# Kernel optimization log

Hardware: AMD Instinct MI355X
Metric: run time of the kernel (lower is better)

## Reference

```python
import jax, jax.numpy as jnp
import numpy as np

N = 4096
IN_F = 256
F = 64      # out_features
H = 4       # heads
NEG_SLOPE = 0.2


def setup_inputs() -> dict:
    key = jax.random.key(0)
    k1, k2, k3, k4 = jax.random.split(key, 4)
    x = jax.random.normal(k1, (N, IN_F), dtype=jnp.float32)
    # symmetric random binary adjacency with self-loops (avoids empty softmax rows)
    adj = jax.random.bernoulli(k2, 0.5, (N, N)).astype(jnp.float32)
    adj = jnp.clip(adj + adj.T, 0.0, 1.0)
    adj = jnp.maximum(adj, jnp.eye(N, dtype=jnp.float32))
    W = jax.random.normal(k3, (IN_F, F * H), dtype=jnp.float32) * (1.0 / np.sqrt(IN_F))
    a = jax.random.normal(k4, (2 * F, 1), dtype=jnp.float32) * 0.1
    return {"x": x, "adj": adj, "W": W, "a": a}


def reference(x, adj, W, a):
    # h: [N, H, F]
    h = (x @ W).reshape(N, H, F)
    # e[i, j, h] = leakyrelu(a_l . h[i, h] + a_r . h[j, h])  -- avoids the O(N^2*H*2F) concat
    a_l = a[:F, 0]
    a_r = a[F:, 0]
    el = jnp.einsum('nhf,f->nh', h, a_l)  # [N, H]
    er = jnp.einsum('nhf,f->nh', h, a_r)  # [N, H]
    e = jax.nn.leaky_relu(el[:, None, :] + er[None, :, :], NEG_SLOPE)  # [N, N, H]
    e = jnp.where(adj[:, :, None] == 0, -jnp.inf, e)
    attention = jax.nn.softmax(e, axis=1)  # softmax over neighbors j
    h_prime = jnp.einsum('ijh,jhf->ihf', attention, h)  # [N, H, F]
    return h_prime.mean(axis=1)  # [N, F]  (heads > 1 -> mean over heads)
```

## Files before the change

kernel.cpp:

```cpp
#include <hip/hip_runtime.h>
#include <hip/hip_bf16.h>

#define NN 4096
#define LOG2E 1.44269504088896340736f
#define SPLITS 16

typedef __attribute__((ext_vector_type(8))) short s8v;
typedef __attribute__((ext_vector_type(4))) float f4v;

__device__ __forceinline__ unsigned fu(float x){ union{float f;unsigned u;}z; z.f=x; return z.u; }
__device__ __forceinline__ unsigned short f2bf_rne(float x){
  unsigned u = fu(x);
  u += 0x7fffu + ((u >> 16) & 1u);
  return (unsigned short)(u >> 16);
}
__device__ __forceinline__ unsigned pack2_rne(float a, float b){
  return (unsigned)f2bf_rne(a) | ((unsigned)f2bf_rne(b) << 16);
}

__global__ __launch_bounds__(256) void k1_proj(
    const float* __restrict__ x, const float* __restrict__ W,
    const float* __restrict__ a, unsigned short* __restrict__ Vf,
    float* __restrict__ el4, float* __restrict__ Qr, float* __restrict__ Sr)
{
  __shared__ float4 xs[512];
  const int t = threadIdx.x;
  const int r0 = blockIdx.x * 8;
  const float4* xg = (const float4*)(x + (size_t)r0 * 256);
  xs[t] = xg[t];
  xs[t + 256] = xg[t + 256];
  __syncthreads();

  float acc[8] = {0.f,0.f,0.f,0.f,0.f,0.f,0.f,0.f};
  const float* Wp = W + t;
  float w0 = Wp[0], w1 = Wp[256], w2 = Wp[512], w3 = Wp[768];
  #pragma unroll 1
  for (int k4 = 0; k4 < 64; ++k4) {
    const int kn = (k4 + 1) & 63;
    float nw0 = Wp[kn*1024 +   0];
    float nw1 = Wp[kn*1024 + 256];
    float nw2 = Wp[kn*1024 + 512];
    float nw3 = Wp[kn*1024 + 768];
    #pragma unroll
    for (int r = 0; r < 8; ++r) {
      float4 xv = xs[r*64 + k4];
      acc[r] = fmaf(xv.x, w0, acc[r]);
      acc[r] = fmaf(xv.y, w1, acc[r]);
      acc[r] = fmaf(xv.z, w2, acc[r]);
      acc[r] = fmaf(xv.w, w3, acc[r]);
    }
    w0 = nw0; w1 = nw1; w2 = nw2; w3 = nw3;
  }

  union { unsigned u[4]; s8v v; } pk;
  #pragma unroll
  for (int p = 0; p < 4; ++p)
    pk.u[p] = pack2_rne(acc[2*p], acc[2*p+1]);
  {
    const int hh = t >> 6, nf = (t >> 4) & 3, mm = t & 15;
    const int jblk = r0 >> 5, qq = (r0 >> 3) & 3;
    const size_t chunk = (size_t)(((hh * 128 + jblk) * 4 + nf) * 64 + qq * 16 + mm);
    *(s8v*)(Vf + chunk * 8) = pk.v;
  }

  const int f = t & 63, h = t >> 6;
  const float al = a[f], ar = a[64 + f];
  #pragma unroll
  for (int r = 0; r < 8; ++r) {
    float v = acc[r] * al;
    float u = acc[r] * ar;
    #pragma unroll
    for (int off = 32; off > 0; off >>= 1) {
      v += __shfl_xor(v, off);
      u += __shfl_xor(u, off);
    }
    if (f == 0) {
      el4[(r0 + r) * 4 + h] = v * LOG2E;
      float up = u * LOG2E;
      Qr[h * NN + (r0 + r)] = __builtin_amdgcn_exp2f(up);
      Sr[h * NN + (r0 + r)] = __builtin_amdgcn_exp2f(0.2f * up);
    }
  }
}

__global__ __launch_bounds__(256) void k0_pack(
    const float* __restrict__ adj, const float* __restrict__ el4,
    const float* __restrict__ Qr, const float* __restrict__ Sr,
    unsigned long long* __restrict__ adjP64,
    float* __restrict__ PL, float* __restrict__ RL)
{
  const int t = threadIdx.x;
  const int w = t >> 6, l = t & 63;
  const int row = blockIdx.x * 4 + w;
  const float* arow = adj + (size_t)row * NN;

  float4 elv = *(const float4*)(el4 + row * 4);
  const float P[4] = { __builtin_amdgcn_exp2f(elv.x), __builtin_amdgcn_exp2f(elv.y),
                       __builtin_amdgcn_exp2f(elv.z), __builtin_amdgcn_exp2f(elv.w) };
  const float R[4] = { __builtin_amdgcn_exp2f(0.2f*elv.x), __builtin_amdgcn_exp2f(0.2f*elv.y),
                       __builtin_amdgcn_exp2f(0.2f*elv.z), __builtin_amdgcn_exp2f(0.2f*elv.w) };
  float lsum[4] = {0.f, 0.f, 0.f, 0.f};

  float af[4], nf_[4];
  #pragma unroll
  for (int k = 0; k < 4; ++k) af[k] = arow[k * 64 + l];

  #pragma unroll 1
  for (int p = 0; p < 16; ++p) {
    const int nbase = (p < 15) ? (p + 1) * 256 : 0;
    #pragma unroll
    for (int k = 0; k < 4; ++k) nf_[k] = arow[nbase + k * 64 + l];

    const int base = p * 256;
    unsigned long long bm[4];
    #pragma unroll
    for (int k = 0; k < 4; ++k) {
      bm[k] = __ballot(af[k] != 0.0f);
      const int j = base + k * 64 + l;
      #pragma unroll
      for (int h = 0; h < 4; ++h) {
        float qv = Qr[h * NN + j];
        float sv = Sr[h * NN + j];
        lsum[h] = fmaf(af[k], fmaxf(P[h] * qv, R[h] * sv), lsum[h]);
      }
    }
    if (l == 0) {
      unsigned long long* dst = adjP64 + (size_t)row * 64 + p * 4;
      dst[0] = bm[0]; dst[1] = bm[1]; dst[2] = bm[2]; dst[3] = bm[3];
    }
    #pragma unroll
    for (int k = 0; k < 4; ++k) af[k] = nf_[k];
  }

  #pragma unroll
  for (int h = 0; h < 4; ++h) {
    float v = lsum[h];
    #pragma unroll
    for (int off = 32; off > 0; off >>= 1) v += __shfl_xor(v, off);
    lsum[h] = v;
  }
  if (l < 4) {
    float li = 1.0f / lsum[l];
    PL[row * 4 + l] = P[l] * li;
    RL[row * 4 + l] = R[l] * li;
  }
}

__global__ __launch_bounds__(256, 4) void k2_attn(
    const unsigned* __restrict__ adjP, const unsigned short* __restrict__ Vf,
    const float* __restrict__ PL, const float* __restrict__ RL,
    const float* __restrict__ Qr, const float* __restrict__ Sr,
    float* __restrict__ accF)
{
  __shared__ float qs[2048];
  const int t = threadIdx.x;
  const int w = t >> 6, l = t & 63;
  const int m = l & 15, q = l >> 4;
  const int i0 = blockIdx.x * 64;
  const int split = blockIdx.y;
  const int i = i0 + w * 16 + m;
  const int jwin = split * 256;

  {
    const int h = t >> 6;
    float4 qv = *(const float4*)(Qr + h * NN + jwin + l * 4);
    float4 sv = *(const float4*)(Sr + h * NN + jwin + l * 4);
    const int jc = l >> 3, qq = (l >> 1) & 3, hp = (l & 1) * 4;
    float* cell = qs + ((h * 8 + jc) * 4 + qq) * 16;
    *(float4*)(cell + hp) = qv;
    *(float4*)(cell + 8 + hp) = sv;
  }

  float4 pl4 = *(const float4*)(PL + i * 4);
  float4 rl4 = *(const float4*)(RL + i * 4);
  const float Pl[4] = {pl4.x, pl4.y, pl4.z, pl4.w};
  const float Rl[4] = {rl4.x, rl4.y, rl4.z, rl4.w};

  union { uint4 v[2]; unsigned u[8]; } aw;
  {
    const uint4* ap = (const uint4*)(adjP + (size_t)i * 128 + split * 8);
    aw.v[0] = ap[0];
    aw.v[1] = ap[1];
  }

  f4v acc[4];
  #pragma unroll
  for (int nf = 0; nf < 4; ++nf) acc[nf] = (f4v){0.f, 0.f, 0.f, 0.f};

  __syncthreads();

  #pragma unroll 1
  for (int jc = 0; jc < 8; ++jc) {
    const unsigned byte = (aw.u[jc] >> (q * 8)) & 0xFFu;
    float bitf[8];
    #pragma unroll
    for (int e = 0; e < 8; ++e)
      bitf[e] = (float)((byte >> e) & 1u);

    #pragma unroll
    for (int h = 0; h < 4; ++h) {
      const float* cell = qs + ((h * 8 + jc) * 4 + q) * 16;
      float4 q0  = *(const float4*)(cell);
      float4 q1  = *(const float4*)(cell + 4);
      float4 sv0 = *(const float4*)(cell + 8);
      float4 sv1 = *(const float4*)(cell + 12);
      const float Ph = Pl[h], Rh = Rl[h];
      float s0 = bitf[0] * fmaxf(Ph * q0.x, Rh * sv0.x);
      float s1 = bitf[1] * fmaxf(Ph * q0.y, Rh * sv0.y);
      float s2 = bitf[2] * fmaxf(Ph * q0.z, Rh * sv0.z);
      float s3 = bitf[3] * fmaxf(Ph * q0.w, Rh * sv0.w);
      float s4 = bitf[4] * fmaxf(Ph * q1.x, Rh * sv1.x);
      float s5 = bitf[5] * fmaxf(Ph * q1.y, Rh * sv1.y);
      float s6 = bitf[6] * fmaxf(Ph * q1.z, Rh * sv1.z);
      float s7 = bitf[7] * fmaxf(Ph * q1.w, Rh * sv1.w);
      union { unsigned u[4]; s8v v; } A;
      A.u[0] = pack2_rne(s0, s1);
      A.u[1] = pack2_rne(s2, s3);
      A.u[2] = pack2_rne(s4, s5);
      A.u[3] = pack2_rne(s6, s7);
      const s8v* vb = (const s8v*)Vf + ((size_t)((h * 128 + split * 8 + jc) * 4)) * 64 + l;
      #pragma unroll
      for (int nf = 0; nf < 4; ++nf) {
        s8v B = vb[nf * 64];
        acc[nf] = __builtin_amdgcn_mfma_f32_16x16x32_bf16(A.v, B, acc[nf], 0, 0, 0);
      }
    }
  }

  const size_t wbase = ((size_t)(split * 64 + blockIdx.x) * 4 + w) * 1024;
  #pragma unroll
  for (int nf = 0; nf < 4; ++nf)
    #pragma unroll
    for (int r = 0; r < 4; ++r)
      accF[wbase + (nf * 4 + r) * 64 + l] = acc[nf][r];
}

__global__ __launch_bounds__(256) void k3_reduce(
    const float* __restrict__ accF, float* __restrict__ out)
{
  const int pos = blockIdx.x * 256 + threadIdx.x;
  float s = 0.f;
  #pragma unroll
  for (int sp = 0; sp < SPLITS; ++sp)
    s += accF[(size_t)sp * 262144 + pos];
  const int l = pos & 63, r = (pos >> 6) & 3, nf = (pos >> 8) & 3;
  const int w = (pos >> 10) & 3, bx = pos >> 12;
  const int row = bx * 64 + w * 16 + (l >> 4) * 4 + r;
  const int col = nf * 16 + (l & 15);
  out[row * 64 + col] = 0.25f * s;
}

extern "C" void kernel_launch(void* const* d_in, const int* in_sizes, int n_in,
                              void* d_out, int out_size, void* d_ws, size_t ws_size,
                              hipStream_t stream) {
  const float* x   = (const float*)d_in[0];
  const float* adj = (const float*)d_in[1];
  const float* W   = (const float*)d_in[2];
  const float* a   = (const float*)d_in[3];
  float* out = (float*)d_out;

  char* ws = (char*)d_ws;
  unsigned short* Vf = (unsigned short*)ws;
  float* el4 = (float*)(ws + (2u << 20));
  float* Qr  = (float*)(ws + (2u << 20) + (64u << 10));
  float* Sr  = (float*)(ws + (2u << 20) + (128u << 10));
  float* PLp = (float*)(ws + (2u << 20) + (192u << 10));
  float* RLp = (float*)(ws + (2u << 20) + (256u << 10));
  unsigned long long* adjP64 = (unsigned long long*)(ws + (2u << 20) + (320u << 10));
  float* accF = (float*)(ws + (4u << 20) + (320u << 10));

  k1_proj<<<512, 256, 0, stream>>>(x, W, a, Vf, el4, Qr, Sr);
  k0_pack<<<1024, 256, 0, stream>>>(adj, el4, Qr, Sr, adjP64, PLp, RLp);
  k2_attn<<<dim3(64, SPLITS), 256, 0, stream>>>((const unsigned*)adjP64, Vf, PLp, RLp,
                                                Qr, Sr, accF);
  k3_reduce<<<1024, 256, 0, stream>>>(accF, out);
}
```

Baseline: 181.3 us.

## Vectorize adjacency packing, prefetch V fragments, replace split reduce with atomics

k0_pack now reads adjacency and Qr/Sr as float4 with one-iteration prefetch, so each 64-bit ballot covers strided columns and the packed bit layout changes. k2_attn decodes the new interleaved bit layout, software-pipelines the V fragment loads one step ahead of the MFMAs, and accumulates the scaled result directly into the output with atomicAdd. This removes the k3_reduce kernel and its partial-sum buffer in exchange for a memset and atomic contention across 16 splits, which also makes the float summation order nondeterministic.

```diff
diff --git a/kernel.cpp b/kernel.cpp
--- a/kernel.cpp
+++ b/kernel.cpp
@@ -83,10 +83,10 @@
   }
 }
 
-__global__ __launch_bounds__(256) void k0_pack(
+__global__ __launch_bounds__(256, 4) void k0_pack(
     const float* __restrict__ adj, const float* __restrict__ el4,
     const float* __restrict__ Qr, const float* __restrict__ Sr,
-    unsigned long long* __restrict__ adjP64,
+    unsigned long long* __restrict__ adjB,
     float* __restrict__ PL, float* __restrict__ RL)
 {
   const int t = threadIdx.x;
@@ -101,35 +101,54 @@
                        __builtin_amdgcn_exp2f(0.2f*elv.z), __builtin_amdgcn_exp2f(0.2f*elv.w) };
   float lsum[4] = {0.f, 0.f, 0.f, 0.f};
 
-  float af[4], nf_[4];
-  #pragma unroll
-  for (int k = 0; k < 4; ++k) af[k] = arow[k * 64 + l];
+  float4 av, qv0, qv1, qv2, qv3, sv0, sv1, sv2, sv3;
+  av  = *(const float4*)(arow + l * 4);
+  qv0 = *(const float4*)(Qr + 0 * NN + l * 4);
+  qv1 = *(const float4*)(Qr + 1 * NN + l * 4);
+  qv2 = *(const float4*)(Qr + 2 * NN + l * 4);
+  qv3 = *(const float4*)(Qr + 3 * NN + l * 4);
+  sv0 = *(const float4*)(Sr + 0 * NN + l * 4);
+  sv1 = *(const float4*)(Sr + 1 * NN + l * 4);
+  sv2 = *(const float4*)(Sr + 2 * NN + l * 4);
+  sv3 = *(const float4*)(Sr + 3 * NN + l * 4);
 
   #pragma unroll 1
   for (int p = 0; p < 16; ++p) {
-    const int nbase = (p < 15) ? (p + 1) * 256 : 0;
-    #pragma unroll
-    for (int k = 0; k < 4; ++k) nf_[k] = arow[nbase + k * 64 + l];
-
-    const int base = p * 256;
-    unsigned long long bm[4];
-    #pragma unroll
-    for (int k = 0; k < 4; ++k) {
-      bm[k] = __ballot(af[k] != 0.0f);
-      const int j = base + k * 64 + l;
-      #pragma unroll
-      for (int h = 0; h < 4; ++h) {
-        float qv = Qr[h * NN + j];
-        float sv = Sr[h * NN + j];
-        lsum[h] = fmaf(af[k], fmaxf(P[h] * qv, R[h] * sv), lsum[h]);
-      }
-    }
+    const int nb = ((p < 15) ? (p + 1) * 256 : 0) + l * 4;
+    float4 nav  = *(const float4*)(arow + nb);
+    float4 nqv0 = *(const float4*)(Qr + 0 * NN + nb);
+    float4 nqv1 = *(const float4*)(Qr + 1 * NN + nb);
+    float4 nqv2 = *(const float4*)(Qr + 2 * NN + nb);
+    float4 nqv3 = *(const float4*)(Qr + 3 * NN + nb);
+    float4 nsv0 = *(const float4*)(Sr + 0 * NN + nb);
+    float4 nsv1 = *(const float4*)(Sr + 1 * NN + nb);
+    float4 nsv2 = *(const float4*)(Sr + 2 * NN + nb);
+    float4 nsv3 = *(const float4*)(Sr + 3 * NN + nb);
+
+    unsigned long long b0 = __ballot(av.x != 0.0f);
+    unsigned long long b1 = __ballot(av.y != 0.0f);
+    unsigned long long b2 = __ballot(av.z != 0.0f);
+    unsigned long long b3 = __ballot(av.w != 0.0f);
     if (l == 0) {
-      unsigned long long* dst = adjP64 + (size_t)row * 64 + p * 4;
-      dst[0] = bm[0]; dst[1] = bm[1]; dst[2] = bm[2]; dst[3] = bm[3];
-    }
-    #pragma unroll
-    for (int k = 0; k < 4; ++k) af[k] = nf_[k];
+      unsigned long long* dst = adjB + (size_t)row * 64 + p * 4;
+      dst[0] = b0; dst[1] = b1; dst[2] = b2; dst[3] = b3;
+    }
+    #pragma unroll
+    for (int h = 0; h < 4; ++h) {
+      const float4 qv = (h==0)?qv0:(h==1)?qv1:(h==2)?qv2:qv3;
+      const float4 sv = (h==0)?sv0:(h==1)?sv1:(h==2)?sv2:sv3;
+      float m0 = fmaxf(P[h] * qv.x, R[h] * sv.x);
+      float m1 = fmaxf(P[h] * qv.y, R[h] * sv.y);
+      float m2 = fmaxf(P[h] * qv.z, R[h] * sv.z);
+      float m3 = fmaxf(P[h] * qv.w, R[h] * sv.w);
+      lsum[h] = fmaf(av.x, m0, lsum[h]);
+      lsum[h] = fmaf(av.y, m1, lsum[h]);
+      lsum[h] = fmaf(av.z, m2, lsum[h]);
+      lsum[h] = fmaf(av.w, m3, lsum[h]);
+    }
+    av = nav;
+    qv0 = nqv0; qv1 = nqv1; qv2 = nqv2; qv3 = nqv3;
+    sv0 = nsv0; sv1 = nsv1; sv2 = nsv2; sv3 = nsv3;
   }
 
   #pragma unroll
@@ -147,10 +166,10 @@
 }
 
 __global__ __launch_bounds__(256, 4) void k2_attn(
-    const unsigned* __restrict__ adjP, const unsigned short* __restrict__ Vf,
+    const unsigned long long* __restrict__ adjB, const unsigned short* __restrict__ Vf,
     const float* __restrict__ PL, const float* __restrict__ RL,
     const float* __restrict__ Qr, const float* __restrict__ Sr,
-    float* __restrict__ accF)
+    float* __restrict__ out)
 {
   __shared__ float qs[2048];
   const int t = threadIdx.x;
@@ -176,29 +195,43 @@
   const float Pl[4] = {pl4.x, pl4.y, pl4.z, pl4.w};
   const float Rl[4] = {rl4.x, rl4.y, rl4.z, rl4.w};
 
-  union { uint4 v[2]; unsigned u[8]; } aw;
-  {
-    const uint4* ap = (const uint4*)(adjP + (size_t)i * 128 + split * 8);
-    aw.v[0] = ap[0];
-    aw.v[1] = ap[1];
-  }
+  const unsigned long long* bp = adjB + (size_t)i * 64 + split * 4;
+  unsigned long long b0 = bp[0], b1 = bp[1], b2 = bp[2], b3 = bp[3];
 
   f4v acc[4];
   #pragma unroll
   for (int nf = 0; nf < 4; ++nf) acc[nf] = (f4v){0.f, 0.f, 0.f, 0.f};
+
+  const s8v* vfp = (const s8v*)Vf;
+  s8v Bc[4];
+  #pragma unroll
+  for (int nf = 0; nf < 4; ++nf)
+    Bc[nf] = vfp[(size_t)((0 * 128 + split * 8 + 0) * 4 + nf) * 64 + l];
 
   __syncthreads();
 
   #pragma unroll 1
   for (int jc = 0; jc < 8; ++jc) {
-    const unsigned byte = (aw.u[jc] >> (q * 8)) & 0xFFu;
+    const unsigned sh = jc * 8 + q * 2;
+    const unsigned t0 = (unsigned)(b0 >> sh) & 3u;
+    const unsigned t1 = (unsigned)(b1 >> sh) & 3u;
+    const unsigned t2 = (unsigned)(b2 >> sh) & 3u;
+    const unsigned t3 = (unsigned)(b3 >> sh) & 3u;
     float bitf[8];
-    #pragma unroll
-    for (int e = 0; e < 8; ++e)
-      bitf[e] = (float)((byte >> e) & 1u);
+    bitf[0] = (float)(t0 & 1u); bitf[4] = (float)(t0 >> 1);
+    bitf[1] = (float)(t1 & 1u); bitf[5] = (float)(t1 >> 1);
+    bitf[2] = (float)(t2 & 1u); bitf[6] = (float)(t2 >> 1);
+    bitf[3] = (float)(t3 & 1u); bitf[7] = (float)(t3 >> 1);
 
     #pragma unroll
     for (int h = 0; h < 4; ++h) {
+      const int hn = (h < 3) ? h + 1 : 0;
+      const int jcn = (h < 3) ? jc : jc + 1;
+      s8v Bn[4];
+      #pragma unroll
+      for (int nf = 0; nf < 4; ++nf)
+        Bn[nf] = vfp[(size_t)((hn * 128 + split * 8 + jcn) * 4 + nf) * 64 + l];
+
       const float* cell = qs + ((h * 8 + jc) * 4 + q) * 16;
       float4 q0  = *(const float4*)(cell);
       float4 q1  = *(const float4*)(cell + 4);
@@ -218,36 +251,22 @@
       A.u[1] = pack2_rne(s2, s3);
       A.u[2] = pack2_rne(s4, s5);
       A.u[3] = pack2_rne(s6, s7);
-      const s8v* vb = (const s8v*)Vf + ((size_t)((h * 128 + split * 8 + jc) * 4)) * 64 + l;
       #pragma unroll
-      for (int nf = 0; nf < 4; ++nf) {
-        s8v B = vb[nf * 64];
-        acc[nf] = __builtin_amdgcn_mfma_f32_16x16x32_bf16(A.v, B, acc[nf], 0, 0, 0);
-      }
-    }
-  }
-
-  const size_t wbase = ((size_t)(split * 64 + blockIdx.x) * 4 + w) * 1024;
+      for (int nf = 0; nf < 4; ++nf)
+        acc[nf] = __builtin_amdgcn_mfma_f32_16x16x32_bf16(A.v, Bc[nf], acc[nf], 0, 0, 0);
+      #pragma unroll
+      for (int nf = 0; nf < 4; ++nf) Bc[nf] = Bn[nf];
+    }
+  }
+
   #pragma unroll
   for (int nf = 0; nf < 4; ++nf)
     #pragma unroll
-    for (int r = 0; r < 4; ++r)
-      accF[wbase + (nf * 4 + r) * 64 + l] = acc[nf][r];
-}
-
-__global__ __launch_bounds__(256) void k3_reduce(
-    const float* __restrict__ accF, float* __restrict__ out)
-{
-  const int pos = blockIdx.x * 256 + threadIdx.x;
-  float s = 0.f;
-  #pragma unroll
-  for (int sp = 0; sp < SPLITS; ++sp)
-    s += accF[(size_t)sp * 262144 + pos];
-  const int l = pos & 63, r = (pos >> 6) & 3, nf = (pos >> 8) & 3;
-  const int w = (pos >> 10) & 3, bx = pos >> 12;
-  const int row = bx * 64 + w * 16 + (l >> 4) * 4 + r;
-  const int col = nf * 16 + (l & 15);
-  out[row * 64 + col] = 0.25f * s;
+    for (int r = 0; r < 4; ++r) {
+      int row = i0 + w * 16 + q * 4 + r;
+      int col = nf * 16 + m;
+      atomicAdd(&out[row * 64 + col], 0.25f * acc[nf][r]);
+    }
 }
 
 extern "C" void kernel_launch(void* const* d_in, const int* in_sizes, int n_in,
@@ -266,12 +285,10 @@
   float* Sr  = (float*)(ws + (2u << 20) + (128u << 10));
   float* PLp = (float*)(ws + (2u << 20) + (192u << 10));
   float* RLp = (float*)(ws + (2u << 20) + (256u << 10));
-  unsigned long long* adjP64 = (unsigned long long*)(ws + (2u << 20) + (320u << 10));
-  float* accF = (float*)(ws + (4u << 20) + (320u << 10));
-
+  unsigned long long* adjB = (unsigned long long*)(ws + (2u << 20) + (320u << 10));
+
+  hipMemsetAsync(out, 0, (size_t)out_size * sizeof(float), stream);
   k1_proj<<<512, 256, 0, stream>>>(x, W, a, Vf, el4, Qr, Sr);
-  k0_pack<<<1024, 256, 0, stream>>>(adj, el4, Qr, Sr, adjP64, PLp, RLp);
-  k2_attn<<<dim3(64, SPLITS), 256, 0, stream>>>((const unsigned*)adjP64, Vf, PLp, RLp,
-                                                Qr, Sr, accF);
-  k3_reduce<<<1024, 256, 0, stream>>>(accF, out);
-}
+  k0_pack<<<1024, 256, 0, stream>>>(adj, el4, Qr, Sr, adjB, PLp, RLp);
+  k2_attn<<<dim3(64, SPLITS), 256, 0, stream>>>(adjB, Vf, PLp, RLp, Qr, Sr, out);
+}
```

Result: faster. 175.4 us (-3.3%).
